# Kernel tuning notes

Measured on AMD Instinct MI355X. Metric: run time of the kernel, lower is better.

The kernel has to match this reference:

```python
import jax, jax.numpy as jnp
import numpy as np

B = 524288
H = 20          # heads
NUM_EX = 13     # embedding rows
EMB = 3         # embedding dim
FEAT_IN, FEAT_OUT = 3, 5
HEAD_IN, HEAD_HID = 8, 10


def setup_inputs() -> dict:
    key = jax.random.key(0)
    ks = jax.random.split(key, 12)
    e = jax.random.randint(ks[0], (B, H), 0, NUM_EX)
    f = jax.random.normal(ks[1], (B, H * FEAT_IN), dtype=jnp.float32)
    # embedding table; row 0 zeroed as in the torch __init__
    emb = jax.random.normal(ks[2], (NUM_EX, EMB), dtype=jnp.float32) * 0.1
    emb = emb.at[0].set(0.0)
    # features Linear(3 -> 5), stored as (in, out) so y = x @ Wf + bf
    Wf = jax.random.normal(ks[3], (FEAT_IN, FEAT_OUT), dtype=jnp.float32) * 0.5
    bf = jax.random.normal(ks[4], (FEAT_OUT,), dtype=jnp.float32) * 0.1
    # 20 parallel head MLPs, batched over the head axis
    W1 = jax.random.normal(ks[5], (H, HEAD_IN, HEAD_HID), dtype=jnp.float32) * 0.3
    b1 = jax.random.normal(ks[6], (H, HEAD_HID), dtype=jnp.float32) * 0.1
    W2 = jax.random.normal(ks[7], (H, HEAD_HID), dtype=jnp.float32) * 0.3
    b2 = jax.random.normal(ks[8], (H,), dtype=jnp.float32) * 0.1
    # output Linear(20 -> 1)
    Wo = jax.random.normal(ks[9], (H, 1), dtype=jnp.float32) * 0.3
    bo = jax.random.normal(ks[10], (1,), dtype=jnp.float32) * 0.1
    return {"e": e, "f": f, "emb": emb, "Wf": Wf, "bf": bf,
            "W1": W1, "b1": b1, "W2": W2, "b2": b2, "Wo": Wo, "bo": bo}


def reference(e, f, emb, Wf, bf, W1, b1, W2, b2, Wo, bo):
    ev = emb[e]                                    # (B, 20, 3) embedding lookup
    fv = f.reshape(-1, H, FEAT_IN) @ Wf + bf       # (B, 20, 5)
    x = jnp.concatenate([ev, fv], axis=2)          # (B, 20, 8)
    # all 20 heads as one batched matmul instead of a Python loop
    h1 = jax.nn.leaky_relu(jnp.einsum('bhi,hio->bho', x, W1) + b1)  # (B, 20, 10)
    h = jax.nn.softplus(jnp.einsum('bho,ho->bh', h1, W2) + b2)      # (B, 20)
    return h @ Wo + bo                             # (B, 1)
```

## Files before the change

kernel.cpp:

```cpp
#include <hip/hip_runtime.h>


#define HH   20
#define NEX  13

__global__ __launch_bounds__(256, 4) void airfit_kernel(
    const int*   __restrict__ e,   const float* __restrict__ f,
    const float* __restrict__ emb, const float* __restrict__ Wf,
    const float* __restrict__ bf,  const float* __restrict__ W1,
    const float* __restrict__ b1,  const float* __restrict__ W2,
    const float* __restrict__ b2,  const float* __restrict__ Wo,
    const float* __restrict__ bo,  float* __restrict__ out, int B)
{
    __shared__ float s_emb[NEX * 4];
    if (threadIdx.x < NEX * 3) {
        int r = threadIdx.x / 3;
        int c = threadIdx.x - r * 3;
        s_emb[r * 4 + c] = emb[threadIdx.x];
    }
    __syncthreads();

    int b = blockIdx.x * 256 + threadIdx.x;
    if (b >= B) return;

    const int4*   ep = reinterpret_cast<const int4*>(e + (size_t)b * HH);
    const float4* fp = reinterpret_cast<const float4*>(f + (size_t)b * (HH * 3));

    float acc = bo[0];

#pragma unroll
    for (int g = 0; g < 5; ++g) {
        int4   iv = ep[g];
        float4 fa = fp[3 * g + 0];
        float4 fb = fp[3 * g + 1];
        float4 fc = fp[3 * g + 2];
        int   ii[4]  = { iv.x, iv.y, iv.z, iv.w };
        float ff[12] = { fa.x, fa.y, fa.z, fa.w,
                         fb.x, fb.y, fb.z, fb.w,
                         fc.x, fc.y, fc.z, fc.w };

#pragma unroll
        for (int j = 0; j < 4; ++j) {
            const int h = 4 * g + j;
            int idx = ii[j];

            float xv[8];
            xv[0] = s_emb[idx * 4 + 0];
            xv[1] = s_emb[idx * 4 + 1];
            xv[2] = s_emb[idx * 4 + 2];

            float g0 = ff[3 * j + 0], g1 = ff[3 * j + 1], g2 = ff[3 * j + 2];
#pragma unroll
            for (int o = 0; o < 5; ++o) {
                float a = bf[o];
                a = fmaf(g0, Wf[0 * 5 + o], a);
                a = fmaf(g1, Wf[1 * 5 + o], a);
                a = fmaf(g2, Wf[2 * 5 + o], a);
                xv[3 + o] = a;
            }

            float hacc = b2[h];
#pragma unroll
            for (int o = 0; o < 10; ++o) {
                float a = b1[h * 10 + o];
#pragma unroll
                for (int i = 0; i < 8; ++i)
                    a = fmaf(xv[i], W1[(h * 8 + i) * 10 + o], a);
                a = fmaxf(a, 0.01f * a);
                hacc = fmaf(a, W2[h * 10 + o], hacc);
            }

            float sp = fmaxf(hacc, 0.0f) + __logf(1.0f + __expf(-fabsf(hacc)));
            acc = fmaf(sp, Wo[h], acc);
        }
    }

    out[b] = acc;
}

extern "C" void kernel_launch(void* const* d_in, const int* in_sizes, int n_in,
                              void* d_out, int out_size, void* d_ws, size_t ws_size,
                              hipStream_t stream) {
    const int*   e   = (const int*)  d_in[0];
    const float* f   = (const float*)d_in[1];
    const float* emb = (const float*)d_in[2];
    const float* Wf  = (const float*)d_in[3];
    const float* bf  = (const float*)d_in[4];
    const float* W1  = (const float*)d_in[5];
    const float* b1  = (const float*)d_in[6];
    const float* W2  = (const float*)d_in[7];
    const float* b2  = (const float*)d_in[8];
    const float* Wo  = (const float*)d_in[9];
    const float* bo  = (const float*)d_in[10];
    float* out = (float*)d_out;

    int B = in_sizes[0] / HH;
    int blocks = (B + 255) / 256;
    airfit_kernel<<<blocks, 256, 0, stream>>>(e, f, emb, Wf, bf, W1, b1,
                                              W2, b2, Wo, bo, out, B);
}
```

Measured before the change: 293.2 us.

## Split 20 heads across 5 wavefronts per item and reduce via LDS

Each block now handles 64 batch items using 320 threads, where each wavefront computes one group of 4 heads for those items. The head group is made wave-uniform with readfirstlane and dispatched to a templated function, so weight addresses are compile-time constants and can be scalar loads. Per-group partial sums are combined through shared memory before the output is written. This gives 5x more threads and less serial work per thread, at the cost of an extra barrier, an LDS reduction, and strided per-wave global loads.

```diff
diff --git a/kernel.cpp b/kernel.cpp
--- a/kernel.cpp
+++ b/kernel.cpp
@@ -4,7 +4,60 @@
 #define HH   20
 #define NEX  13
 
-__global__ __launch_bounds__(256, 4) void airfit_kernel(
+__device__ __forceinline__ float softplus_fast(float x) {
+    return fmaxf(x, 0.0f) + __logf(1.0f + __expf(-fabsf(x)));
+}
+
+template<int J>
+__device__ __forceinline__ float head_group(
+    int4 iv, float4 fa, float4 fb, float4 fc,
+    const float4* __restrict__ s_emb,
+    const float* __restrict__ Wf, const float* __restrict__ bf,
+    const float* __restrict__ W1, const float* __restrict__ b1,
+    const float* __restrict__ W2, const float* __restrict__ b2,
+    const float* __restrict__ Wo)
+{
+    int   ii[4]  = { iv.x, iv.y, iv.z, iv.w };
+    float ff[12] = { fa.x, fa.y, fa.z, fa.w,
+                     fb.x, fb.y, fb.z, fb.w,
+                     fc.x, fc.y, fc.z, fc.w };
+    float partial = 0.0f;
+
+#pragma unroll
+    for (int t = 0; t < 4; ++t) {
+        const int h = 4 * J + t;
+        float4 ev = s_emb[ii[t]];
+
+        float xv[8];
+        xv[0] = ev.x; xv[1] = ev.y; xv[2] = ev.z;
+
+        float g0 = ff[3 * t + 0], g1 = ff[3 * t + 1], g2 = ff[3 * t + 2];
+#pragma unroll
+        for (int o = 0; o < 5; ++o) {
+            float a = bf[o];
+            a = fmaf(g0, Wf[0 * 5 + o], a);
+            a = fmaf(g1, Wf[1 * 5 + o], a);
+            a = fmaf(g2, Wf[2 * 5 + o], a);
+            xv[3 + o] = a;
+        }
+
+        float hacc = b2[h];
+#pragma unroll
+        for (int o = 0; o < 10; ++o) {
+            float a = b1[h * 10 + o];
+#pragma unroll
+            for (int k = 0; k < 8; ++k)
+                a = fmaf(xv[k], W1[(h * 8 + k) * 10 + o], a);
+            a = fmaxf(a, 0.01f * a);
+            hacc = fmaf(a, W2[h * 10 + o], hacc);
+        }
+
+        partial = fmaf(softplus_fast(hacc), Wo[h], partial);
+    }
+    return partial;
+}
+
+__global__ __launch_bounds__(320, 6) void airfit_kernel(
     const int*   __restrict__ e,   const float* __restrict__ f,
     const float* __restrict__ emb, const float* __restrict__ Wf,
     const float* __restrict__ bf,  const float* __restrict__ W1,
@@ -12,70 +65,44 @@
     const float* __restrict__ b2,  const float* __restrict__ Wo,
     const float* __restrict__ bo,  float* __restrict__ out, int B)
 {
-    __shared__ float s_emb[NEX * 4];
-    if (threadIdx.x < NEX * 3) {
-        int r = threadIdx.x / 3;
-        int c = threadIdx.x - r * 3;
-        s_emb[r * 4 + c] = emb[threadIdx.x];
+    __shared__ float4 s_emb[NEX];
+    __shared__ float  s_part[5][64];
+
+    if (threadIdx.x < NEX) {
+        int r = threadIdx.x;
+        s_emb[r] = make_float4(emb[3 * r + 0], emb[3 * r + 1],
+                               emb[3 * r + 2], 0.0f);
     }
     __syncthreads();
 
-    int b = blockIdx.x * 256 + threadIdx.x;
-    if (b >= B) return;
+    const int i    = threadIdx.x & 63;
+    const int jj   = threadIdx.x >> 6;
+    const int item = blockIdx.x * 64 + i;
 
-    const int4*   ep = reinterpret_cast<const int4*>(e + (size_t)b * HH);
-    const float4* fp = reinterpret_cast<const float4*>(f + (size_t)b * (HH * 3));
+    if (item < B) {
+        int4 iv = *(reinterpret_cast<const int4*>(e + (size_t)item * HH) + jj);
+        const float4* fp =
+            reinterpret_cast<const float4*>(f + (size_t)item * (HH * 3)) + 3 * jj;
+        float4 fa = fp[0], fb = fp[1], fc = fp[2];
 
-    float acc = bo[0];
+        const int j = __builtin_amdgcn_readfirstlane(jj);
+        float partial;
+        switch (j) {
+        case 0:  partial = head_group<0>(iv, fa, fb, fc, s_emb, Wf, bf, W1, b1, W2, b2, Wo); break;
+        case 1:  partial = head_group<1>(iv, fa, fb, fc, s_emb, Wf, bf, W1, b1, W2, b2, Wo); break;
+        case 2:  partial = head_group<2>(iv, fa, fb, fc, s_emb, Wf, bf, W1, b1, W2, b2, Wo); break;
+        case 3:  partial = head_group<3>(iv, fa, fb, fc, s_emb, Wf, bf, W1, b1, W2, b2, Wo); break;
+        default: partial = head_group<4>(iv, fa, fb, fc, s_emb, Wf, bf, W1, b1, W2, b2, Wo); break;
+        }
+        s_part[jj][i] = partial;
+    }
+    __syncthreads();
 
-#pragma unroll
-    for (int g = 0; g < 5; ++g) {
-        int4   iv = ep[g];
-        float4 fa = fp[3 * g + 0];
-        float4 fb = fp[3 * g + 1];
-        float4 fc = fp[3 * g + 2];
-        int   ii[4]  = { iv.x, iv.y, iv.z, iv.w };
-        float ff[12] = { fa.x, fa.y, fa.z, fa.w,
-                         fb.x, fb.y, fb.z, fb.w,
-                         fc.x, fc.y, fc.z, fc.w };
-
-#pragma unroll
-        for (int j = 0; j < 4; ++j) {
-            const int h = 4 * g + j;
-            int idx = ii[j];
-
-            float xv[8];
-            xv[0] = s_emb[idx * 4 + 0];
-            xv[1] = s_emb[idx * 4 + 1];
-            xv[2] = s_emb[idx * 4 + 2];
-
-            float g0 = ff[3 * j + 0], g1 = ff[3 * j + 1], g2 = ff[3 * j + 2];
-#pragma unroll
-            for (int o = 0; o < 5; ++o) {
-                float a = bf[o];
-                a = fmaf(g0, Wf[0 * 5 + o], a);
-                a = fmaf(g1, Wf[1 * 5 + o], a);
-                a = fmaf(g2, Wf[2 * 5 + o], a);
-                xv[3 + o] = a;
-            }
-
-            float hacc = b2[h];
-#pragma unroll
-            for (int o = 0; o < 10; ++o) {
-                float a = b1[h * 10 + o];
-#pragma unroll
-                for (int i = 0; i < 8; ++i)
-                    a = fmaf(xv[i], W1[(h * 8 + i) * 10 + o], a);
-                a = fmaxf(a, 0.01f * a);
-                hacc = fmaf(a, W2[h * 10 + o], hacc);
-            }
-
-            float sp = fmaxf(hacc, 0.0f) + __logf(1.0f + __expf(-fabsf(hacc)));
-            acc = fmaf(sp, Wo[h], acc);
-        }
+    if (jj == 0 && item < B) {
+        float r = bo[0] + s_part[0][i] + s_part[1][i] + s_part[2][i]
+                        + s_part[3][i] + s_part[4][i];
+        out[item] = r;
     }
-
-    out[b] = acc;
 }
 
 extern "C" void kernel_launch(void* const* d_in, const int* in_sizes, int n_in,
@@ -95,7 +122,7 @@
     float* out = (float*)d_out;
 
     int B = in_sizes[0] / HH;
-    int blocks = (B + 255) / 256;
-    airfit_kernel<<<blocks, 256, 0, stream>>>(e, f, emb, Wf, bf, W1, b1,
+    int blocks = (B + 63) / 64;
+    airfit_kernel<<<blocks, 320, 0, stream>>>(e, f, emb, Wf, bf, W1, b1,
                                               W2, b2, Wo, bo, out, B);
 }
```

New measurement: 269.3 us. 1.09x faster.
